# Kernel tuning notes

Measured on AMD Instinct MI355X. Metric: run time of the kernel, lower is better.

## Reference

```python
import jax, jax.numpy as jnp
import numpy as np

BLOCK = 64
THRESH = 0.95
EPS = 1e-8


def setup_inputs() -> dict:
    key = jax.random.key(0)
    kq, kk, kv = jax.random.split(key, 3)
    S, D = 4096, 128
    q = jax.random.normal(kq, (S, D), dtype=jnp.float32)
    k = jax.random.normal(kk, (S, D), dtype=jnp.float32)
    v = jax.random.normal(kv, (S, D), dtype=jnp.float32)
    return {"q": q, "k": k, "v": v}


def reference(q, k, v):
    S, D = q.shape
    nb = S // BLOCK
    qb = q.reshape(nb, BLOCK, D)
    kb = k.reshape(nb, BLOCK, D)
    vb = v.reshape(nb, BLOCK, D)
    # all block-pair scores: [nb_q, nb_k, BLOCK_q, BLOCK_k]
    scores = jnp.einsum('ibd,jcd->ijbc', qb, kb)
    m = jnp.max(scores, axis=-1, keepdims=True)
    e = jnp.exp(scores - m)
    s = jnp.sum(e, axis=-1, keepdims=True)  # per-block-pair softmax denominator
    # top-p truncation mask: sort descending, cumsum, threshold
    srt = jnp.sort(e, axis=-1)[..., ::-1]
    cum = jnp.cumsum(srt, axis=-1)
    mask = cum < THRESH * s
    # NOTE: faithful to original — mask (in sorted order) is applied to the
    # UNSORTED exp_scores, exactly as the torch code does (indices unused).
    em = e * mask
    em = em / (jnp.sum(em, axis=-1, keepdims=True) + EPS)
    # accumulate over key blocks j (per-pair normalized weights, summed)
    out = jnp.einsum('ijbc,jcd->ibd', em, vb)
    return out.reshape(S, D)
```

## Files before the change

### kernel.cpp

```cpp
#include <hip/hip_runtime.h>
#include <cstdint>
#include <cstddef>


#define SEQ   4096
#define DIM   128
#define BLK   64
#define NB    (SEQ / BLK)
#define NJG   16
#define JPB   (NB / NJG)
#define NT    256
#define PSTR  12288
#define THRESH 0.95f
#define EPSF   1e-8f
#define PPART  (PSTR * NB)
#define PARTF  (NJG * SEQ * DIM)
#define WS_NEED ((size_t)PPART * 4 + (size_t)PARTF * 4)

typedef __attribute__((ext_vector_type(8))) _Float16 f16x8;
typedef __attribute__((ext_vector_type(4))) float    f32x4;

#define MFMAH(a, b, c) __builtin_amdgcn_mfma_f32_16x16x32_f16((a), (b), (c), 0, 0, 0)

union UH4 { uint2 u; _Float16 h[4]; };
union UH8 { uint4 u; f16x8 v; };

__device__ __forceinline__ void gll16(const uint* g, uint* l) {
  __builtin_amdgcn_global_load_lds(
      (const __attribute__((address_space(1))) void*)g,
      (__attribute__((address_space(3))) void*)l, 16, 0, 0);
}

template <bool ZERO>
__global__ __launch_bounds__(NT, 4) void eco_prep_kernel(
    const float* __restrict__ K, const float* __restrict__ V,
    uint* __restrict__ P, float* __restrict__ O) {
  const int tid = threadIdx.x;
  const int w   = blockIdx.x;
  const int jb  = w >> 4;
  const int sub = w & 15;

  if (tid < 128) {
    if constexpr (ZERO) {
      float4 z = {0.f, 0.f, 0.f, 0.f};
      ((float4*)O)[w * 128 + tid] = z;
    }

    const float4* gk = (const float4*)(K + (size_t)jb * BLK * DIM);
    uint* dst = P + (size_t)jb * PSTR;
    int f = sub * 128 + tid;
    int r = f >> 5, c4 = f & 31;
    int nt = r >> 4, q = (r >> 2) & 3, rg = r & 3;
    int pi = (q << 3) | ((nt & 1) << 5) | ((nt >> 1) << 2) | rg;
    float4 x = gk[pi * 32 + c4];
    float xs[4] = {x.x, x.y, x.z, x.w};
    UH4 uh, ur;
#pragma unroll
    for (int e = 0; e < 4; ++e) {
      float v = xs[e];
      _Float16 h = (_Float16)v;
      uh.h[e] = h;
      ur.h[e] = (_Float16)(v - (float)h);
    }
    uint off = (uint)r * 64u + (((uint)(c4 >> 1) ^ (uint)(r & 15)) << 2) +
               (uint)((c4 & 1) << 1);
    *(uint2*)&dst[off]        = uh.u;
    *(uint2*)&dst[4096 + off] = ur.u;
  } else if (tid < 192) {
    const float* gv = V + (size_t)jb * BLK * DIM;
    uint4* dv = (uint4*)(P + (size_t)jb * PSTR + 8192);
    int idx = sub * 64 + (tid - 128);
    int ch = idx >> 7, d = idx & 127;
    UH8 u;
#pragma unroll
    for (int j = 0; j < 8; ++j)
      u.v[j] = (_Float16)gv[(ch * 8 + j) * DIM + d];
    dv[idx] = u.u;
  }
}

__global__ __launch_bounds__(NT) void eco_reduce_kernel(
    const float* __restrict__ Part, float* __restrict__ O) {
  const int gid = blockIdx.x * NT + threadIdx.x;
  const float4* p4 = (const float4*)Part;
  float4 a = p4[gid];
#pragma unroll
  for (int jg = 1; jg < NJG; ++jg) {
    float4 b = p4[(size_t)jg * (SEQ * DIM / 4) + gid];
    a.x += b.x; a.y += b.y; a.z += b.z; a.w += b.w;
  }
  ((float4*)O)[gid] = a;
}

template <bool PARTIAL>
__global__ __launch_bounds__(NT, 4) void eco_attn_kernel(
    const float* __restrict__ Q, const uint* __restrict__ P,
    float* __restrict__ O, float* __restrict__ Part) {
  __shared__ __align__(16) uint sK[8192];

  const int tid  = threadIdx.x;
  const int ib   = blockIdx.y;
  const int jg   = blockIdx.x;
  const int lane = tid & 63;
  const int wv   = tid >> 6;
  const int quad = lane >> 4;
  const int l16  = lane & 15;
  const int q8   = quad << 3;

  f16x8 qh[4], qr[4];
  {
    const float* qp = Q + (size_t)(ib * BLK + wv * 16 + l16) * DIM + quad * 8;
#pragma unroll
    for (int ks = 0; ks < 4; ++ks) {
      float4 x0 = *(const float4*)(qp + ks * 32);
      float4 x1 = *(const float4*)(qp + ks * 32 + 4);
      float xs[8] = {x0.x, x0.y, x0.z, x0.w, x1.x, x1.y, x1.z, x1.w};
      f16x8 h8, r8;
#pragma unroll
      for (int e = 0; e < 8; ++e) {
        float v = xs[e];
        _Float16 h = (_Float16)v;
        h8[e] = h;
        r8[e] = (_Float16)(v - (float)h);
      }
      qh[ks] = h8; qr[ks] = r8;
    }
  }

  const f32x4 zf = {0.f, 0.f, 0.f, 0.f};
  f32x4 pv[8];
#pragma unroll
  for (int i = 0; i < 8; ++i) pv[i] = zf;

  {
    const uint* gsrc = P + (size_t)(jg * JPB) * PSTR;
#pragma unroll
    for (int it = 0; it < 8; ++it) {
      int idx = (it * NT + tid) << 2;
      gll16(gsrc + idx, sK + idx);
    }
  }

  for (int jj = 0; jj < JPB; ++jj) {
    const int jb = jg * JPB + jj;
    __syncthreads();

    f32x4 acc[4];
#pragma unroll
    for (int nt = 0; nt < 4; ++nt) acc[nt] = zf;
#pragma unroll
    for (int nt = 0; nt < 4; ++nt) {
      const int rB = nt * 16 + l16;
      const uint rowoff = (uint)rB * 64u;
      const uint swk = (uint)(rB & 15);
#pragma unroll
      for (int ks = 0; ks < 4; ++ks) {
        uint off = rowoff + ((((uint)(ks * 4 + quad)) ^ swk) << 2);
        f16x8 bh = *(const f16x8*)&sK[off];
        f16x8 br = *(const f16x8*)&sK[4096 + off];
        acc[nt] = MFMAH(bh, qh[ks], acc[nt]);
        acc[nt] = MFMAH(br, qh[ks], acc[nt]);
        acc[nt] = MFMAH(bh, qr[ks], acc[nt]);
      }
    }
    __syncthreads();

    if (jj + 1 < JPB) {
      const uint* gsrc = P + (size_t)(jb + 1) * PSTR;
#pragma unroll
      for (int it = 0; it < 8; ++it) {
        int idx = (it * NT + tid) << 2;
        gll16(gsrc + idx, sK + idx);
      }
    }

    const uint* gvt = P + (size_t)jb * PSTR + 8192;

    bool doHi;
    f16x8 wf0, wf1;

    {
      float a[16], e[16];
#pragma unroll
      for (int nt = 0; nt < 4; ++nt) {
#pragma unroll
        for (int rg = 0; rg < 4; ++rg) a[nt * 4 + rg] = acc[nt][rg];
      }
      float mt[8];
#pragma unroll
      for (int i = 0; i < 8; ++i) mt[i] = fmaxf(a[i], a[i + 8]);
#pragma unroll
      for (int w2 = 4; w2 >= 1; w2 >>= 1)
#pragma unroll
        for (int i = 0; i < w2; ++i) mt[i] = fmaxf(mt[i], mt[i + w2]);
      float m = mt[0];
      m = fmaxf(m, __shfl_xor(m, 16, 64));
      m = fmaxf(m, __shfl_xor(m, 32, 64));
#pragma unroll
      for (int i = 0; i < 16; ++i) { a[i] = __expf(a[i] - m); e[i] = a[i]; }
      float st[8];
#pragma unroll
      for (int i = 0; i < 8; ++i) st[i] = a[i] + a[i + 8];
#pragma unroll
      for (int w2 = 4; w2 >= 1; w2 >>= 1)
#pragma unroll
        for (int i = 0; i < w2; ++i) st[i] += st[i + w2];
      float sr = st[0];
      sr += __shfl_xor(sr, 16, 64);
      sr += __shfl_xor(sr, 32, 64);
      const float T = THRESH * sr;

      float cum = 1.0f;
      bool live = (cum < T);
      int t = live ? 1 : 0;
#pragma unroll
      for (int i = 0; i < 16; ++i) a[i] = (a[i] >= 1.0f) ? 0.f : a[i];
#pragma unroll
      for (int p4 = 0; p4 < 4; ++p4) {
        float M = fmaxf(fmaxf(fmaxf(a[0], a[1]), a[2]),
                        fmaxf(fmaxf(a[3], a[4]), a[5]));
        M = fmaxf(M, fmaxf(fmaxf(a[6],  a[7]),  a[8]));
        M = fmaxf(M, fmaxf(fmaxf(a[9],  a[10]), a[11]));
        M = fmaxf(M, fmaxf(fmaxf(a[12], a[13]), a[14]));
        M = fmaxf(M, a[15]);
        M = fmaxf(M, __shfl_xor(M, 16, 64));
        M = fmaxf(M, __shfl_xor(M, 32, 64));
        const float cn = cum + M;
        const bool cross = !(cn < T) || !(M > 0.f);
        if (live) { cum = cn; t += cross ? 0 : 1; }
        live = live && !cross;
#pragma unroll
        for (int i = 0; i < 16; ++i) a[i] = (a[i] >= M) ? 0.f : a[i];
      }

      while (__any(live)) {
        float M = fmaxf(fmaxf(fmaxf(a[0], a[1]), a[2]),
                        fmaxf(fmaxf(a[3], a[4]), a[5]));
        M = fmaxf(M, fmaxf(fmaxf(a[6],  a[7]),  a[8]));
        M = fmaxf(M, fmaxf(fmaxf(a[9],  a[10]), a[11]));
        M = fmaxf(M, fmaxf(fmaxf(a[12], a[13]), a[14]));
        M = fmaxf(M, a[15]);
        M = fmaxf(M, __shfl_xor(M, 16, 64));
        M = fmaxf(M, __shfl_xor(M, 32, 64));
        const float cn = cum + M;
        const bool cross = !(cn < T) || !(M > 0.f);
        if (live) { cum = cn; t += cross ? 0 : 1; }
        live = live && !cross;
#pragma unroll
        for (int i = 0; i < 16; ++i) a[i] = (a[i] >= M) ? 0.f : a[i];
      }

      doHi = __any(t > 32);

      float p = 0.f;
#pragma unroll
      for (int i = 0; i < 16; ++i) {
        int kidx = q8 + (((i >> 2) & 1) << 5) + ((i >> 3) << 2) + (i & 3);
        p += (kidx < t) ? e[i] : 0.f;
      }
      p += __shfl_xor(p, 16, 64);
      p += __shfl_xor(p, 32, 64);
      const float rn = 1.0f / (p + EPSF);

      {
        UH8 w0;
#pragma unroll
        for (int j = 0; j < 8; ++j) {
          int i0 = ((j >> 2) << 3) + (j & 3);
          int k0 = q8 + j;
          w0.v[j] = (_Float16)((k0 < t) ? e[i0] * rn : 0.f);
        }
        wf0 = w0.v;
      }
      if (doHi) {
        UH8 w1;
#pragma unroll
        for (int j = 0; j < 8; ++j) {
          int i1 = 4 + ((j >> 2) << 3) + (j & 3);
          int k1 = q8 + 32 + j;
          w1.v[j] = (_Float16)((k1 < t) ? e[i1] * rn : 0.f);
        }
        wf1 = w1.v;
      }
    }

    {
#pragma unroll
      for (int nt2 = 0; nt2 < 8; ++nt2) {
        f16x8 vf = *(const f16x8*)&gvt[((uint)(quad * 128 +
                                               nt2 * 16 + l16)) << 2];
        pv[nt2] = MFMAH(wf0, vf, pv[nt2]);
      }
    }
    if (doHi) {
#pragma unroll
      for (int nt2 = 0; nt2 < 8; ++nt2) {
        f16x8 vf = *(const f16x8*)&gvt[((uint)((4 + quad) * 128 +
                                               nt2 * 16 + l16)) << 2];
        pv[nt2] = MFMAH(wf1, vf, pv[nt2]);
      }
    }
  }

  if constexpr (PARTIAL) {
    float* pb = Part + (size_t)jg * (SEQ * DIM);
    const int row0 = ib * BLK + wv * 16 + quad * 4;
#pragma unroll
    for (int nt2 = 0; nt2 < 8; ++nt2) {
      const int col = nt2 * 16 + l16;
#pragma unroll
      for (int rg = 0; rg < 4; ++rg)
        pb[(size_t)(row0 + rg) * DIM + col] = pv[nt2][rg];
    }
  } else {
#pragma unroll
    for (int nt2 = 0; nt2 < 8; ++nt2) {
      const int col  = nt2 * 16 + l16;
      const int row0 = ib * BLK + wv * 16 + quad * 4;
#pragma unroll
      for (int rg = 0; rg < 4; ++rg)
        atomicAdd(O + (size_t)(row0 + rg) * DIM + col, pv[nt2][rg]);
    }
  }
}

extern "C" void kernel_launch(void* const* d_in, const int* in_sizes, int n_in,
                              void* d_out, int out_size, void* d_ws, size_t ws_size,
                              hipStream_t stream) {
  (void)in_sizes; (void)n_in; (void)out_size;
  const float* q = (const float*)d_in[0];
  const float* k = (const float*)d_in[1];
  const float* v = (const float*)d_in[2];
  float* out = (float*)d_out;
  uint* prep = (uint*)d_ws;
  float* part = (float*)((char*)d_ws + (size_t)PPART * 4);

  if (ws_size >= WS_NEED) {
    eco_prep_kernel<false><<<dim3(NB * 16), dim3(NT), 0, stream>>>(k, v, prep, out);
    eco_attn_kernel<true><<<dim3(NJG, NB), dim3(NT), 0, stream>>>(q, prep, out, part);
    eco_reduce_kernel<<<dim3(SEQ * DIM / 4 / NT), dim3(NT), 0, stream>>>(part, out);
  } else {
    eco_prep_kernel<true><<<dim3(NB * 16), dim3(NT), 0, stream>>>(k, v, prep, out);
    eco_attn_kernel<false><<<dim3(NJG, NB), dim3(NT), 0, stream>>>(q, prep, out, nullptr);
  }
}
```

Measured before the change: 98.04 us.

## Fuse partial-sum reduction into attention kernel via last-block counter

Removes the separate reduce kernel launch. Each attention block now atomically bumps a per-query-block counter after writing its partial, and the last of the NJG blocks sums all partials for that row block and writes the output. The counter is zeroed in the prep kernel. This saves one kernel launch and its tail, at the cost of a threadfence, extra syncs, and serialized reduction work on the final block of each row.

```diff
diff --git a/kernel.cpp b/kernel.cpp
--- a/kernel.cpp
+++ b/kernel.cpp
@@ -15,7 +15,7 @@
 #define EPSF   1e-8f
 #define PPART  (PSTR * NB)
 #define PARTF  (NJG * SEQ * DIM)
-#define WS_NEED ((size_t)PPART * 4 + (size_t)PARTF * 4)
+#define WS_NEED ((size_t)PPART * 4 + (size_t)PARTF * 4 + (size_t)NB * 4)
 
 typedef __attribute__((ext_vector_type(8))) _Float16 f16x8;
 typedef __attribute__((ext_vector_type(4))) float    f32x4;
@@ -34,11 +34,15 @@
 template <bool ZERO>
 __global__ __launch_bounds__(NT, 4) void eco_prep_kernel(
     const float* __restrict__ K, const float* __restrict__ V,
-    uint* __restrict__ P, float* __restrict__ O) {
+    uint* __restrict__ P, float* __restrict__ O, int* __restrict__ Cnt) {
   const int tid = threadIdx.x;
   const int w   = blockIdx.x;
   const int jb  = w >> 4;
   const int sub = w & 15;
+
+  if constexpr (!ZERO) {
+    if (w == 0 && tid < NB) Cnt[tid] = 0;
+  }
 
   if (tid < 128) {
     if constexpr (ZERO) {
@@ -79,23 +83,10 @@
   }
 }
 
-__global__ __launch_bounds__(NT) void eco_reduce_kernel(
-    const float* __restrict__ Part, float* __restrict__ O) {
-  const int gid = blockIdx.x * NT + threadIdx.x;
-  const float4* p4 = (const float4*)Part;
-  float4 a = p4[gid];
-#pragma unroll
-  for (int jg = 1; jg < NJG; ++jg) {
-    float4 b = p4[(size_t)jg * (SEQ * DIM / 4) + gid];
-    a.x += b.x; a.y += b.y; a.z += b.z; a.w += b.w;
-  }
-  ((float4*)O)[gid] = a;
-}
-
 template <bool PARTIAL>
 __global__ __launch_bounds__(NT, 4) void eco_attn_kernel(
     const float* __restrict__ Q, const uint* __restrict__ P,
-    float* __restrict__ O, float* __restrict__ Part) {
+    float* __restrict__ O, float* __restrict__ Part, int* __restrict__ Cnt) {
   __shared__ __align__(16) uint sK[8192];
 
   const int tid  = threadIdx.x;
@@ -312,6 +303,30 @@
       for (int rg = 0; rg < 4; ++rg)
         pb[(size_t)(row0 + rg) * DIM + col] = pv[nt2][rg];
     }
+    __threadfence();
+    __syncthreads();
+    if (tid == 0) {
+      int old = atomicAdd(Cnt + ib, 1);
+      ((volatile int*)sK)[0] = (old == NJG - 1) ? 1 : 0;
+    }
+    __syncthreads();
+    if (((volatile int*)sK)[0] != 0) {
+      __threadfence();
+      const float4* p4 = (const float4*)Part;
+      float4* o4 = (float4*)O;
+      const int base = ib * (BLK * DIM / 4);
+#pragma unroll
+      for (int it = 0; it < (BLK * DIM / 4) / NT; ++it) {
+        const int idx = base + it * NT + tid;
+        float4 a = p4[idx];
+#pragma unroll
+        for (int jg2 = 1; jg2 < NJG; ++jg2) {
+          float4 b = p4[(size_t)jg2 * (SEQ * DIM / 4) + idx];
+          a.x += b.x; a.y += b.y; a.z += b.z; a.w += b.w;
+        }
+        o4[idx] = a;
+      }
+    }
   } else {
 #pragma unroll
     for (int nt2 = 0; nt2 < 8; ++nt2) {
@@ -334,13 +349,13 @@
   float* out = (float*)d_out;
   uint* prep = (uint*)d_ws;
   float* part = (float*)((char*)d_ws + (size_t)PPART * 4);
+  int* cnt = (int*)((char*)d_ws + (size_t)PPART * 4 + (size_t)PARTF * 4);
 
   if (ws_size >= WS_NEED) {
-    eco_prep_kernel<false><<<dim3(NB * 16), dim3(NT), 0, stream>>>(k, v, prep, out);
-    eco_attn_kernel<true><<<dim3(NJG, NB), dim3(NT), 0, stream>>>(q, prep, out, part);
-    eco_reduce_kernel<<<dim3(SEQ * DIM / 4 / NT), dim3(NT), 0, stream>>>(part, out);
+    eco_prep_kernel<false><<<dim3(NB * 16), dim3(NT), 0, stream>>>(k, v, prep, out, cnt);
+    eco_attn_kernel<true><<<dim3(NJG, NB), dim3(NT), 0, stream>>>(q, prep, out, part, cnt);
   } else {
-    eco_prep_kernel<true><<<dim3(NB * 16), dim3(NT), 0, stream>>>(k, v, prep, out);
-    eco_attn_kernel<false><<<dim3(NJG, NB), dim3(NT), 0, stream>>>(q, prep, out, nullptr);
+    eco_prep_kernel<true><<<dim3(NB * 16), dim3(NT), 0, stream>>>(k, v, prep, out, cnt);
+    eco_attn_kernel<false><<<dim3(NJG, NB), dim3(NT), 0, stream>>>(q, prep, out, nullptr, cnt);
   }
 }
```

After: 274.6 us. +180.1%, slower.
